# Performance work log

Hardware: AMD Instinct MI355X
Metric: run time of the kernel (lower is better)

Reference implementation:

```python
import jax, jax.numpy as jnp
import numpy as np

HEAD_SIZE = 64


def setup_inputs() -> dict:
    key = jax.random.key(0)
    k1, k2, k3, k4 = jax.random.split(key, 4)
    B, T, E = 8, 2048, 1024
    x = jax.random.normal(k1, (B, T, E), dtype=jnp.float32)
    # nn.Linear(n_embd, head_size, bias=False) weights: [head_size, n_embd]
    s = 1.0 / np.sqrt(E)
    Wk = jax.random.uniform(k2, (HEAD_SIZE, E), jnp.float32, -s, s)
    Wq = jax.random.uniform(k3, (HEAD_SIZE, E), jnp.float32, -s, s)
    Wv = jax.random.uniform(k4, (HEAD_SIZE, E), jnp.float32, -s, s)
    return {"x": x, "Wk": Wk, "Wq": Wq, "Wv": Wv}


def reference(x, Wk, Wq, Wv):
    # x: [B, T, E]; W*: [D, E] with D = head_size
    B, T, E = x.shape
    k = jnp.einsum("bte,de->btd", x, Wk)  # [B,T,D]
    q = jnp.einsum("bte,de->btd", x, Wq)
    v = jnp.einsum("bte,de->btd", x, Wv)
    scale = k.shape[-1] ** -0.5
    wei = jnp.einsum("btd,bsd->bts", q, k) * scale  # [B,T,T]
    causal = jnp.tril(jnp.ones((T, T), dtype=bool))
    wei = jnp.where(causal, wei, -jnp.inf)
    wei = jax.nn.softmax(wei, axis=-1)
    # dropout p=0.0 (eval): identity
    return jnp.einsum("bts,bsd->btd", wei, v)
```

## Files before the change

kernel.cpp:

```cpp
#include <hip/hip_runtime.h>
#include <hip/hip_bf16.h>


typedef __bf16 bf16x8 __attribute__((ext_vector_type(8)));
typedef float  f32x4  __attribute__((ext_vector_type(4)));

#define T_SEQ 2048
#define E_DIM 1024
#define D_HEAD 64
#define M_TOT 16384

__device__ __forceinline__ unsigned short f2b(float f) {
  union { float f; unsigned int u; } cv; cv.f = f;
  unsigned int u = cv.u;
  u += 0x7FFFu + ((u >> 16) & 1u);
  return (unsigned short)(u >> 16);
}

__device__ __forceinline__ void dma16(const unsigned short* g, unsigned short* l) {
  __builtin_amdgcn_global_load_lds(
      (const __attribute__((address_space(1))) void*)g,
      (__attribute__((address_space(3))) void*)l, 16, 0, 0);
}

__global__ __launch_bounds__(256) void wcvt_kernel(
    const float* __restrict__ Wk, const float* __restrict__ Wq,
    const float* __restrict__ Wv, unsigned short* __restrict__ Wb)
{
  int i = blockIdx.x * 256 + threadIdx.x;
  int n = i >> 8, c4 = i & 255;
  const float* src = (n < 64) ? Wq + n * E_DIM
                   : (n < 128) ? Wk + (n - 64) * E_DIM
                               : Wv + (n - 128) * E_DIM;
  float4 v = *(const float4*)(src + c4 * 4);
  *(ushort4*)(Wb + (size_t)n * E_DIM + c4 * 4) =
      make_ushort4(f2b(v.x), f2b(v.y), f2b(v.z), f2b(v.w));
}

__global__ __launch_bounds__(256) void proj_kernel(
    const float* __restrict__ x, const unsigned short* __restrict__ Wb,
    unsigned short* __restrict__ qws, unsigned short* __restrict__ kws,
    unsigned short* __restrict__ vtws)
{
  __shared__ unsigned short x_lds[32 * 128];
  __shared__ unsigned short w_lds[192 * 128];

  const int tid = threadIdx.x, wv = tid >> 6, lane = tid & 63;
  const int c = lane & 15, quad = lane >> 4;
  const int row0 = blockIdx.x * 32;
  const int mi = wv & 1, nh = wv >> 1;

  f32x4 acc[6];
  for (int j = 0; j < 6; ++j)
    for (int r = 0; r < 4; ++r) acc[j][r] = 0.0f;

  for (int step = 0; step < 8; ++step) {
    const int k0 = step * 128;
    __syncthreads();
    for (int jj = 0; jj < 4; ++jj) {
      int idx = tid + jj * 256;
      int r = idx >> 5, h = idx & 31;
      float4 v = *(const float4*)(x + (size_t)(row0 + r) * E_DIM + k0 + h * 4);
      int pc = (h >> 1) ^ (r & 7);
      *(ushort4*)&x_lds[r * 128 + pc * 8 + (h & 1) * 4] =
          make_ushort4(f2b(v.x), f2b(v.y), f2b(v.z), f2b(v.w));
    }
    for (int j = 0; j < 12; ++j) {
      int base = (wv * 12 + j) * 64;
      int p = base + lane;
      int n = p >> 4, pg = p & 15, g = pg ^ (n & 7);
      dma16(Wb + (size_t)n * E_DIM + k0 + g * 8, &w_lds[base * 8]);
    }
    __syncthreads();
    const int m = mi * 16 + c;
    for (int ks = 0; ks < 4; ++ks) {
      int ga = (ks * 4 + quad) ^ (m & 7);
      bf16x8 a = *(const bf16x8*)&x_lds[m * 128 + ga * 8];
      for (int j = 0; j < 6; ++j) {
        int n = (nh * 6 + j) * 16 + c;
        int gb = (ks * 4 + quad) ^ (n & 7);
        bf16x8 bb = *(const bf16x8*)&w_lds[n * 128 + gb * 8];
        acc[j] = __builtin_amdgcn_mfma_f32_16x16x32_bf16(a, bb, acc[j], 0, 0, 0);
      }
    }
  }

  const int rbase = row0 + mi * 16 + quad * 4;
  for (int j = 0; j < 6; ++j) {
    int nt = nh * 6 + j;
    if (nt < 4) {
      int d = nt * 16 + c;
      for (int r = 0; r < 4; ++r) qws[(size_t)(rbase + r) * D_HEAD + d] = f2b(acc[j][r]);
    } else if (nt < 8) {
      int d = (nt - 4) * 16 + c;
      for (int r = 0; r < 4; ++r) kws[(size_t)(rbase + r) * D_HEAD + d] = f2b(acc[j][r]);
    } else {
      int d = (nt - 8) * 16 + c;
      int bb = rbase >> 11, tt = rbase & 2047;
      *(ushort4*)&vtws[(size_t)bb * D_HEAD * T_SEQ + (size_t)d * T_SEQ + tt] =
          make_ushort4(f2b(acc[j][0]), f2b(acc[j][1]), f2b(acc[j][2]), f2b(acc[j][3]));
    }
  }
}

__global__ __launch_bounds__(256) void attn_kernel(
    const unsigned short* __restrict__ qws, const unsigned short* __restrict__ kws,
    const unsigned short* __restrict__ vtws,
    float* __restrict__ opart, float* __restrict__ mpart, float* __restrict__ lpart)
{
  __shared__ unsigned short q_lds[64 * 64];
  __shared__ unsigned short k_lds[128 * 64];
  __shared__ unsigned short vt_lds[64 * 128];
  __shared__ unsigned short p_lds[64 * 128];

  const int tid = threadIdx.x, wv = tid >> 6, lane = tid & 63;
  const int c = lane & 15, quad = lane >> 4;
  const int qt = blockIdx.x, b = blockIdx.y, sg = blockIdx.z;
  const int t0 = qt * 64;
  const size_t qkbase = (size_t)b * T_SEQ * D_HEAD;
  const int ssmax = qt >> 1;
  const int niter = (ssmax >= sg) ? ((ssmax - sg) >> 1) + 1 : 0;
  const int rloc = wv * 16 + quad * 4;
  const size_t prow = ((size_t)sg * 8 + b) * T_SEQ;

  if (niter == 0) {
    for (int nt = 0; nt < 4; ++nt)
      for (int r = 0; r < 4; ++r)
        opart[(prow + t0 + rloc + r) * D_HEAD + nt * 16 + c] = 0.0f;
    if (c == 0)
      for (int r = 0; r < 4; ++r) {
        mpart[prow + t0 + rloc + r] = -__builtin_inff();
        lpart[prow + t0 + rloc + r] = 0.0f;
      }
    return;
  }

  for (int j = 0; j < 2; ++j) {
    int base = (wv * 2 + j) * 64;
    int p = base + lane;
    int r = p >> 3, pg = p & 7, g = pg ^ (r & 7);
    dma16(qws + qkbase + (size_t)(t0 + r) * D_HEAD + g * 8, &q_lds[base * 8]);
  }

  float m_st[4], l_st[4];
  f32x4 acc_o[4];
  for (int r = 0; r < 4; ++r) { m_st[r] = -__builtin_inff(); l_st[r] = 0.0f; }
  for (int nt = 0; nt < 4; ++nt)
    for (int r = 0; r < 4; ++r) acc_o[nt][r] = 0.0f;

  const float sc = 0.18033688011112042f;
  const int m_row = wv * 16 + c;

  for (int it = 0; it < niter; ++it) {
    const int ss = sg + 2 * it;
    const int s0 = ss * 128;
    __syncthreads();
    for (int j = 0; j < 4; ++j) {
      int base = (wv * 4 + j) * 64;
      int p = base + lane;
      int r = p >> 3, pg = p & 7, g = pg ^ (r & 7);
      dma16(kws + qkbase + (size_t)(s0 + r) * D_HEAD + g * 8, &k_lds[base * 8]);
    }
    for (int j = 0; j < 4; ++j) {
      int base = (wv * 4 + j) * 64;
      int p = base + lane;
      int r = p >> 4, pg = p & 15, g = pg ^ (r & 7);
      dma16(vtws + (size_t)b * D_HEAD * T_SEQ + (size_t)r * T_SEQ + s0 + g * 8,
            &vt_lds[base * 8]);
    }
    __syncthreads();

    f32x4 accs[8];
    for (int nt = 0; nt < 8; ++nt)
      for (int r = 0; r < 4; ++r) accs[nt][r] = 0.0f;
    for (int ks = 0; ks < 2; ++ks) {
      int ga = (ks * 4 + quad) ^ (m_row & 7);
      bf16x8 a = *(const bf16x8*)&q_lds[m_row * 64 + ga * 8];
      for (int nt = 0; nt < 8; ++nt) {
        int n = nt * 16 + c;
        int gb = (ks * 4 + quad) ^ (n & 7);
        bf16x8 bb = *(const bf16x8*)&k_lds[n * 64 + gb * 8];
        accs[nt] = __builtin_amdgcn_mfma_f32_16x16x32_bf16(a, bb, accs[nt], 0, 0, 0);
      }
    }
    for (int nt = 0; nt < 8; ++nt)
      for (int r = 0; r < 4; ++r) accs[nt][r] *= sc;
    if (ss == ssmax) {
      for (int nt = 0; nt < 8; ++nt) {
        int scol = s0 + nt * 16 + c;
        for (int r = 0; r < 4; ++r)
          if (scol > t0 + rloc + r) accs[nt][r] = -__builtin_inff();
      }
    }

    float mx[4];
    for (int r = 0; r < 4; ++r) {
      float v = accs[0][r];
      for (int nt = 1; nt < 8; ++nt) v = fmaxf(v, accs[nt][r]);
      mx[r] = v;
    }
    for (int off = 1; off < 16; off <<= 1)
      for (int r = 0; r < 4; ++r) mx[r] = fmaxf(mx[r], __shfl_xor(mx[r], off));
    float alpha[4], rsum[4];
    for (int r = 0; r < 4; ++r) {
      float mnew = fmaxf(m_st[r], mx[r]);
      alpha[r] = __builtin_exp2f(m_st[r] - mnew);
      m_st[r] = mnew;
      rsum[r] = 0.0f;
    }
    for (int nt = 0; nt < 8; ++nt)
      for (int r = 0; r < 4; ++r) {
        float p = __builtin_exp2f(accs[nt][r] - m_st[r]);
        accs[nt][r] = p;
        rsum[r] += p;
      }
    for (int off = 1; off < 16; off <<= 1)
      for (int r = 0; r < 4; ++r) rsum[r] += __shfl_xor(rsum[r], off);
    for (int r = 0; r < 4; ++r) l_st[r] = alpha[r] * l_st[r] + rsum[r];
    for (int nt = 0; nt < 4; ++nt)
      for (int r = 0; r < 4; ++r) acc_o[nt][r] *= alpha[r];

    for (int nt = 0; nt < 8; ++nt)
      for (int r = 0; r < 4; ++r) {
        int col = nt * 16 + c, rr = rloc + r;
        int pc = (col >> 3) ^ (rr & 7);
        p_lds[rr * 128 + pc * 8 + (col & 7)] = f2b(accs[nt][r]);
      }

    for (int ks = 0; ks < 4; ++ks) {
      int ga = (ks * 4 + quad) ^ (m_row & 7);
      bf16x8 a = *(const bf16x8*)&p_lds[m_row * 128 + ga * 8];
      for (int nt = 0; nt < 4; ++nt) {
        int n = nt * 16 + c;
        int gb = (ks * 4 + quad) ^ (n & 7);
        bf16x8 vv = *(const bf16x8*)&vt_lds[n * 128 + gb * 8];
        acc_o[nt] = __builtin_amdgcn_mfma_f32_16x16x32_bf16(a, vv, acc_o[nt], 0, 0, 0);
      }
    }
  }

  for (int nt = 0; nt < 4; ++nt)
    for (int r = 0; r < 4; ++r)
      opart[(prow + t0 + rloc + r) * D_HEAD + nt * 16 + c] = acc_o[nt][r];
  if (c == 0)
    for (int r = 0; r < 4; ++r) {
      mpart[prow + t0 + rloc + r] = m_st[r];
      lpart[prow + t0 + rloc + r] = l_st[r];
    }
}

__global__ __launch_bounds__(256) void merge_kernel(
    const float* __restrict__ opart, const float* __restrict__ mpart,
    const float* __restrict__ lpart, float* __restrict__ out)
{
  int gid = blockIdx.x * 256 + threadIdx.x;
  int gr = gid >> 4, q4 = gid & 15;
  float m0 = mpart[gr], m1 = mpart[M_TOT + gr];
  float l0 = lpart[gr], l1 = lpart[M_TOT + gr];
  float M = fmaxf(m0, m1);
  float w0 = __builtin_exp2f(m0 - M);
  float w1 = __builtin_exp2f(m1 - M);
  float inv = 1.0f / (w0 * l0 + w1 * l1);
  const float4 o0 = *(const float4*)(opart + (size_t)gr * D_HEAD + q4 * 4);
  const float4 o1 = *(const float4*)(opart + (size_t)M_TOT * D_HEAD + (size_t)gr * D_HEAD + q4 * 4);
  float4 o;
  o.x = (w0 * o0.x + w1 * o1.x) * inv;
  o.y = (w0 * o0.y + w1 * o1.y) * inv;
  o.z = (w0 * o0.z + w1 * o1.z) * inv;
  o.w = (w0 * o0.w + w1 * o1.w) * inv;
  *(float4*)(out + (size_t)gr * D_HEAD + q4 * 4) = o;
}

extern "C" void kernel_launch(void* const* d_in, const int* in_sizes, int n_in,
                              void* d_out, int out_size, void* d_ws, size_t ws_size,
                              hipStream_t stream) {
  const float* x  = (const float*)d_in[0];
  const float* Wk = (const float*)d_in[1];
  const float* Wq = (const float*)d_in[2];
  const float* Wv = (const float*)d_in[3];
  float* out = (float*)d_out;

  unsigned short* qws  = (unsigned short*)d_ws;
  unsigned short* kws  = qws + (size_t)M_TOT * D_HEAD;
  unsigned short* vtws = kws + (size_t)M_TOT * D_HEAD;
  unsigned short* Wb   = vtws + (size_t)M_TOT * D_HEAD;
  float* opart = (float*)(Wb + 192 * E_DIM);
  float* mpart = opart + 2 * (size_t)M_TOT * D_HEAD;
  float* lpart = mpart + 2 * (size_t)M_TOT;

  wcvt_kernel<<<192, 256, 0, stream>>>(Wk, Wq, Wv, Wb);
  proj_kernel<<<M_TOT / 32, 256, 0, stream>>>(x, Wb, qws, kws, vtws);
  attn_kernel<<<dim3(T_SEQ / 64, 8, 2), 256, 0, stream>>>(qws, kws, vtws, opart, mpart, lpart);
  merge_kernel<<<M_TOT * 16 / 256, 256, 0, stream>>>(opart, mpart, lpart, out);
}
```

Measured before the change: 144.8 us.

## Rewrite projection and attention to load fragments directly from global, split KV four ways

```diff
diff --git a/kernel.cpp b/kernel.cpp
--- a/kernel.cpp
+++ b/kernel.cpp
@@ -9,6 +9,8 @@
 #define E_DIM 1024
 #define D_HEAD 64
 #define M_TOT 16384
+#define NSPLIT 4
+#define SC_LOG2E 0.18033688011112042f
 
 __device__ __forceinline__ unsigned short f2b(float f) {
   union { float f; unsigned int u; } cv; cv.f = f;
@@ -17,10 +19,15 @@
   return (unsigned short)(u >> 16);
 }
 
-__device__ __forceinline__ void dma16(const unsigned short* g, unsigned short* l) {
-  __builtin_amdgcn_global_load_lds(
-      (const __attribute__((address_space(1))) void*)g,
-      (__attribute__((address_space(3))) void*)l, 16, 0, 0);
+__device__ __forceinline__ unsigned int f2b2(float a, float b) {
+#if __has_builtin(__builtin_amdgcn_cvt_pk_bf16_f32)
+  typedef __bf16 bf16x2_t __attribute__((ext_vector_type(2)));
+  union { bf16x2_t v; unsigned int u; } cv;
+  cv.v = __builtin_amdgcn_cvt_pk_bf16_f32(a, b);
+  return cv.u;
+#else
+  return (unsigned int)f2b(a) | ((unsigned int)f2b(b) << 16);
+#endif
 }
 
 __global__ __launch_bounds__(256) void wcvt_kernel(
@@ -33,100 +40,94 @@
                    : (n < 128) ? Wk + (n - 64) * E_DIM
                                : Wv + (n - 128) * E_DIM;
   float4 v = *(const float4*)(src + c4 * 4);
-  *(ushort4*)(Wb + (size_t)n * E_DIM + c4 * 4) =
-      make_ushort4(f2b(v.x), f2b(v.y), f2b(v.z), f2b(v.w));
-}
-
-__global__ __launch_bounds__(256) void proj_kernel(
+  unsigned int lo = f2b2(v.x, v.y), hi = f2b2(v.z, v.w);
+  *(uint2*)(Wb + (size_t)n * E_DIM + c4 * 4) = make_uint2(lo, hi);
+}
+
+__global__ __launch_bounds__(192) void proj_kernel(
     const float* __restrict__ x, const unsigned short* __restrict__ Wb,
     unsigned short* __restrict__ qws, unsigned short* __restrict__ kws,
     unsigned short* __restrict__ vtws)
 {
-  __shared__ unsigned short x_lds[32 * 128];
-  __shared__ unsigned short w_lds[192 * 128];
-
-  const int tid = threadIdx.x, wv = tid >> 6, lane = tid & 63;
+  const int tid = threadIdx.x, wv = tid / 64, lane = tid & 63;
   const int c = lane & 15, quad = lane >> 4;
-  const int row0 = blockIdx.x * 32;
-  const int mi = wv & 1, nh = wv >> 1;
-
-  f32x4 acc[6];
-  for (int j = 0; j < 6; ++j)
-    for (int r = 0; r < 4; ++r) acc[j][r] = 0.0f;
-
-  for (int step = 0; step < 8; ++step) {
-    const int k0 = step * 128;
-    __syncthreads();
-    for (int jj = 0; jj < 4; ++jj) {
-      int idx = tid + jj * 256;
-      int r = idx >> 5, h = idx & 31;
-      float4 v = *(const float4*)(x + (size_t)(row0 + r) * E_DIM + k0 + h * 4);
-      int pc = (h >> 1) ^ (r & 7);
-      *(ushort4*)&x_lds[r * 128 + pc * 8 + (h & 1) * 4] =
-          make_ushort4(f2b(v.x), f2b(v.y), f2b(v.z), f2b(v.w));
-    }
-    for (int j = 0; j < 12; ++j) {
-      int base = (wv * 12 + j) * 64;
-      int p = base + lane;
-      int n = p >> 4, pg = p & 15, g = pg ^ (n & 7);
-      dma16(Wb + (size_t)n * E_DIM + k0 + g * 8, &w_lds[base * 8]);
-    }
-    __syncthreads();
-    const int m = mi * 16 + c;
-    for (int ks = 0; ks < 4; ++ks) {
-      int ga = (ks * 4 + quad) ^ (m & 7);
-      bf16x8 a = *(const bf16x8*)&x_lds[m * 128 + ga * 8];
-      for (int j = 0; j < 6; ++j) {
-        int n = (nh * 6 + j) * 16 + c;
-        int gb = (ks * 4 + quad) ^ (n & 7);
-        bf16x8 bb = *(const bf16x8*)&w_lds[n * 128 + gb * 8];
-        acc[j] = __builtin_amdgcn_mfma_f32_16x16x32_bf16(a, bb, acc[j], 0, 0, 0);
-      }
-    }
-  }
-
-  const int rbase = row0 + mi * 16 + quad * 4;
-  for (int j = 0; j < 6; ++j) {
-    int nt = nh * 6 + j;
-    if (nt < 4) {
-      int d = nt * 16 + c;
-      for (int r = 0; r < 4; ++r) qws[(size_t)(rbase + r) * D_HEAD + d] = f2b(acc[j][r]);
-    } else if (nt < 8) {
-      int d = (nt - 4) * 16 + c;
-      for (int r = 0; r < 4; ++r) kws[(size_t)(rbase + r) * D_HEAD + d] = f2b(acc[j][r]);
+  const int mt0 = blockIdx.x * 2;
+  const int ng = wv;
+  const size_t xr0 = (size_t)(mt0 * 16 + c) * E_DIM + quad * 8;
+  const size_t xr1 = xr0 + 16 * E_DIM;
+
+  f32x4 acc0[4], acc1[4];
+  for (int j = 0; j < 4; ++j)
+    for (int r = 0; r < 4; ++r) { acc0[j][r] = 0.0f; acc1[j][r] = 0.0f; }
+
+  for (int k = 0; k < E_DIM; k += 32) {
+    union { unsigned int u32[4]; bf16x8 v8; } a0, a1;
+    {
+      float4 u = *(const float4*)(x + xr0 + k);
+      float4 w = *(const float4*)(x + xr0 + k + 4);
+      a0.u32[0] = f2b2(u.x, u.y); a0.u32[1] = f2b2(u.z, u.w);
+      a0.u32[2] = f2b2(w.x, w.y); a0.u32[3] = f2b2(w.z, w.w);
+    }
+    {
+      float4 u = *(const float4*)(x + xr1 + k);
+      float4 w = *(const float4*)(x + xr1 + k + 4);
+      a1.u32[0] = f2b2(u.x, u.y); a1.u32[1] = f2b2(u.z, u.w);
+      a1.u32[2] = f2b2(w.x, w.y); a1.u32[3] = f2b2(w.z, w.w);
+    }
+    for (int j = 0; j < 4; ++j) {
+      bf16x8 bb = *(const bf16x8*)(Wb + (size_t)(ng * 64 + j * 16 + c) * E_DIM + k + quad * 8);
+      acc0[j] = __builtin_amdgcn_mfma_f32_16x16x32_bf16(a0.v8, bb, acc0[j], 0, 0, 0);
+      acc1[j] = __builtin_amdgcn_mfma_f32_16x16x32_bf16(a1.v8, bb, acc1[j], 0, 0, 0);
+    }
+  }
+
+  for (int half = 0; half < 2; ++half) {
+    const f32x4* acc = half ? acc1 : acc0;
+    const int rbase = (mt0 + half) * 16 + quad * 4;
+    if (ng == 0) {
+      for (int j = 0; j < 4; ++j) {
+        int d = j * 16 + c;
+        for (int r = 0; r < 4; ++r)
+          qws[(size_t)(rbase + r) * D_HEAD + d] = f2b(acc[j][r] * SC_LOG2E);
+      }
+    } else if (ng == 1) {
+      for (int j = 0; j < 4; ++j) {
+        int d = j * 16 + c;
+        for (int r = 0; r < 4; ++r)
+          kws[(size_t)(rbase + r) * D_HEAD + d] = f2b(acc[j][r]);
+      }
     } else {
-      int d = (nt - 8) * 16 + c;
       int bb = rbase >> 11, tt = rbase & 2047;
-      *(ushort4*)&vtws[(size_t)bb * D_HEAD * T_SEQ + (size_t)d * T_SEQ + tt] =
-          make_ushort4(f2b(acc[j][0]), f2b(acc[j][1]), f2b(acc[j][2]), f2b(acc[j][3]));
-    }
-  }
-}
-
-__global__ __launch_bounds__(256) void attn_kernel(
+      for (int j = 0; j < 4; ++j) {
+        int d = j * 16 + c;
+        *(ushort4*)&vtws[(size_t)bb * D_HEAD * T_SEQ + (size_t)d * T_SEQ + tt] =
+            make_ushort4(f2b(acc[j][0]), f2b(acc[j][1]), f2b(acc[j][2]), f2b(acc[j][3]));
+      }
+    }
+  }
+}
+
+__global__ __launch_bounds__(256, 4) void attn_kernel(
     const unsigned short* __restrict__ qws, const unsigned short* __restrict__ kws,
     const unsigned short* __restrict__ vtws,
-    float* __restrict__ opart, float* __restrict__ mpart, float* __restrict__ lpart)
-{
-  __shared__ unsigned short q_lds[64 * 64];
-  __shared__ unsigned short k_lds[128 * 64];
-  __shared__ unsigned short vt_lds[64 * 128];
-  __shared__ unsigned short p_lds[64 * 128];
+    unsigned short* __restrict__ opart, float* __restrict__ mpart,
+    float* __restrict__ lpart)
+{
+  __shared__ __align__(16) unsigned short p_lds[64 * 64];
 
   const int tid = threadIdx.x, wv = tid >> 6, lane = tid & 63;
   const int c = lane & 15, quad = lane >> 4;
   const int qt = blockIdx.x, b = blockIdx.y, sg = blockIdx.z;
   const int t0 = qt * 64;
-  const size_t qkbase = (size_t)b * T_SEQ * D_HEAD;
-  const int ssmax = qt >> 1;
-  const int niter = (ssmax >= sg) ? ((ssmax - sg) >> 1) + 1 : 0;
+  const size_t qkb = (size_t)b * T_SEQ * D_HEAD;
+  const int niter = (qt >= sg) ? ((qt - sg) >> 2) + 1 : 0;
   const int rloc = wv * 16 + quad * 4;
   const size_t prow = ((size_t)sg * 8 + b) * T_SEQ;
 
   if (niter == 0) {
     for (int nt = 0; nt < 4; ++nt)
       for (int r = 0; r < 4; ++r)
-        opart[(prow + t0 + rloc + r) * D_HEAD + nt * 16 + c] = 0.0f;
+        opart[(prow + t0 + rloc + r) * D_HEAD + nt * 16 + c] = 0;
     if (c == 0)
       for (int r = 0; r < 4; ++r) {
         mpart[prow + t0 + rloc + r] = -__builtin_inff();
@@ -135,58 +136,39 @@
     return;
   }
 
-  for (int j = 0; j < 2; ++j) {
-    int base = (wv * 2 + j) * 64;
-    int p = base + lane;
-    int r = p >> 3, pg = p & 7, g = pg ^ (r & 7);
-    dma16(qws + qkbase + (size_t)(t0 + r) * D_HEAD + g * 8, &q_lds[base * 8]);
-  }
-
-  float m_st[4], l_st[4];
-  f32x4 acc_o[4];
-  for (int r = 0; r < 4; ++r) { m_st[r] = -__builtin_inff(); l_st[r] = 0.0f; }
+  const int mrow = wv * 16 + c;
+  const bf16x8 qf0 = *(const bf16x8*)(qws + qkb + (size_t)(t0 + mrow) * D_HEAD + quad * 8);
+  const bf16x8 qf1 = *(const bf16x8*)(qws + qkb + (size_t)(t0 + mrow) * D_HEAD + 32 + quad * 8);
+
+  bf16x8 ones;
+  { union { unsigned short s[8]; bf16x8 v; } o;
+    for (int i = 0; i < 8; ++i) o.s[i] = 0x3F80;
+    ones = o.v; }
+
+  float m_st[4];
+  f32x4 acc_o[4], acc_l;
+  for (int r = 0; r < 4; ++r) { m_st[r] = -__builtin_inff(); acc_l[r] = 0.0f; }
   for (int nt = 0; nt < 4; ++nt)
     for (int r = 0; r < 4; ++r) acc_o[nt][r] = 0.0f;
 
-  const float sc = 0.18033688011112042f;
-  const int m_row = wv * 16 + c;
+  const bool mydiag = (sg == (qt & 3));
 
   for (int it = 0; it < niter; ++it) {
-    const int ss = sg + 2 * it;
-    const int s0 = ss * 128;
-    __syncthreads();
-    for (int j = 0; j < 4; ++j) {
-      int base = (wv * 4 + j) * 64;
-      int p = base + lane;
-      int r = p >> 3, pg = p & 7, g = pg ^ (r & 7);
-      dma16(kws + qkbase + (size_t)(s0 + r) * D_HEAD + g * 8, &k_lds[base * 8]);
-    }
-    for (int j = 0; j < 4; ++j) {
-      int base = (wv * 4 + j) * 64;
-      int p = base + lane;
-      int r = p >> 4, pg = p & 15, g = pg ^ (r & 7);
-      dma16(vtws + (size_t)b * D_HEAD * T_SEQ + (size_t)r * T_SEQ + s0 + g * 8,
-            &vt_lds[base * 8]);
-    }
-    __syncthreads();
-
-    f32x4 accs[8];
-    for (int nt = 0; nt < 8; ++nt)
+    const int s0 = (sg + 4 * it) * 64;
+    const bool diag = mydiag && (it == niter - 1);
+
+    f32x4 accs[4];
+    for (int nt = 0; nt < 4; ++nt)
       for (int r = 0; r < 4; ++r) accs[nt][r] = 0.0f;
-    for (int ks = 0; ks < 2; ++ks) {
-      int ga = (ks * 4 + quad) ^ (m_row & 7);
-      bf16x8 a = *(const bf16x8*)&q_lds[m_row * 64 + ga * 8];
-      for (int nt = 0; nt < 8; ++nt) {
-        int n = nt * 16 + c;
-        int gb = (ks * 4 + quad) ^ (n & 7);
-        bf16x8 bb = *(const bf16x8*)&k_lds[n * 64 + gb * 8];
-        accs[nt] = __builtin_amdgcn_mfma_f32_16x16x32_bf16(a, bb, accs[nt], 0, 0, 0);
-      }
-    }
-    for (int nt = 0; nt < 8; ++nt)
-      for (int r = 0; r < 4; ++r) accs[nt][r] *= sc;
-    if (ss == ssmax) {
-      for (int nt = 0; nt < 8; ++nt) {
+    for (int nt = 0; nt < 4; ++nt) {
+      const unsigned short* kp = kws + qkb + (size_t)(s0 + nt * 16 + c) * D_HEAD + quad * 8;
+      bf16x8 k0 = *(const bf16x8*)kp;
+      bf16x8 k1 = *(const bf16x8*)(kp + 32);
+      accs[nt] = __builtin_amdgcn_mfma_f32_16x16x32_bf16(qf0, k0, accs[nt], 0, 0, 0);
+      accs[nt] = __builtin_amdgcn_mfma_f32_16x16x32_bf16(qf1, k1, accs[nt], 0, 0, 0);
+    }
+    if (diag) {
+      for (int nt = 0; nt < 4; ++nt) {
         int scol = s0 + nt * 16 + c;
         for (int r = 0; r < 4; ++r)
           if (scol > t0 + rloc + r) accs[nt][r] = -__builtin_inff();
@@ -194,81 +176,75 @@
     }
 
     float mx[4];
-    for (int r = 0; r < 4; ++r) {
-      float v = accs[0][r];
-      for (int nt = 1; nt < 8; ++nt) v = fmaxf(v, accs[nt][r]);
-      mx[r] = v;
-    }
+    for (int r = 0; r < 4; ++r)
+      mx[r] = fmaxf(fmaxf(accs[0][r], accs[1][r]), fmaxf(accs[2][r], accs[3][r]));
     for (int off = 1; off < 16; off <<= 1)
       for (int r = 0; r < 4; ++r) mx[r] = fmaxf(mx[r], __shfl_xor(mx[r], off));
-    float alpha[4], rsum[4];
+    float alpha[4];
     for (int r = 0; r < 4; ++r) {
       float mnew = fmaxf(m_st[r], mx[r]);
       alpha[r] = __builtin_exp2f(m_st[r] - mnew);
       m_st[r] = mnew;
-      rsum[r] = 0.0f;
-    }
-    for (int nt = 0; nt < 8; ++nt)
+    }
+    for (int nt = 0; nt < 4; ++nt)
+      for (int r = 0; r < 4; ++r)
+        accs[nt][r] = __builtin_exp2f(accs[nt][r] - m_st[r]);
+    for (int r = 0; r < 4; ++r) acc_l[r] *= alpha[r];
+    for (int nt = 0; nt < 4; ++nt)
+      for (int r = 0; r < 4; ++r) acc_o[nt][r] *= alpha[r];
+
+    for (int nt = 0; nt < 4; ++nt)
       for (int r = 0; r < 4; ++r) {
-        float p = __builtin_exp2f(accs[nt][r] - m_st[r]);
-        accs[nt][r] = p;
-        rsum[r] += p;
-      }
-    for (int off = 1; off < 16; off <<= 1)
-      for (int r = 0; r < 4; ++r) rsum[r] += __shfl_xor(rsum[r], off);
-    for (int r = 0; r < 4; ++r) l_st[r] = alpha[r] * l_st[r] + rsum[r];
-    for (int nt = 0; nt < 4; ++nt)
-      for (int r = 0; r < 4; ++r) acc_o[nt][r] *= alpha[r];
-
-    for (int nt = 0; nt < 8; ++nt)
-      for (int r = 0; r < 4; ++r) {
-        int col = nt * 16 + c, rr = rloc + r;
-        int pc = (col >> 3) ^ (rr & 7);
-        p_lds[rr * 128 + pc * 8 + (col & 7)] = f2b(accs[nt][r]);
-      }
-
-    for (int ks = 0; ks < 4; ++ks) {
-      int ga = (ks * 4 + quad) ^ (m_row & 7);
-      bf16x8 a = *(const bf16x8*)&p_lds[m_row * 128 + ga * 8];
+        int rr = rloc + r;
+        p_lds[rr * 64 + (((nt * 2 + (c >> 3)) ^ (rr & 7)) << 3) + (c & 7)] = f2b(accs[nt][r]);
+      }
+
+    for (int ks = 0; ks < 2; ++ks) {
+      int kg = ks * 4 + quad;
+      bf16x8 pf = *(const bf16x8*)&p_lds[mrow * 64 + ((kg ^ (mrow & 7)) << 3)];
+      acc_l = __builtin_amdgcn_mfma_f32_16x16x32_bf16(pf, ones, acc_l, 0, 0, 0);
       for (int nt = 0; nt < 4; ++nt) {
-        int n = nt * 16 + c;
-        int gb = (ks * 4 + quad) ^ (n & 7);
-        bf16x8 vv = *(const bf16x8*)&vt_lds[n * 128 + gb * 8];
-        acc_o[nt] = __builtin_amdgcn_mfma_f32_16x16x32_bf16(a, vv, acc_o[nt], 0, 0, 0);
+        const bf16x8 vv = *(const bf16x8*)(vtws + (size_t)b * D_HEAD * T_SEQ +
+                                           (size_t)(nt * 16 + c) * T_SEQ + s0 + ks * 32 + quad * 8);
+        acc_o[nt] = __builtin_amdgcn_mfma_f32_16x16x32_bf16(pf, vv, acc_o[nt], 0, 0, 0);
       }
     }
   }
 
   for (int nt = 0; nt < 4; ++nt)
     for (int r = 0; r < 4; ++r)
-      opart[(prow + t0 + rloc + r) * D_HEAD + nt * 16 + c] = acc_o[nt][r];
+      opart[(prow + t0 + rloc + r) * D_HEAD + nt * 16 + c] = f2b(acc_o[nt][r]);
   if (c == 0)
     for (int r = 0; r < 4; ++r) {
       mpart[prow + t0 + rloc + r] = m_st[r];
-      lpart[prow + t0 + rloc + r] = l_st[r];
+      lpart[prow + t0 + rloc + r] = acc_l[r];
     }
 }
 
 __global__ __launch_bounds__(256) void merge_kernel(
-    const float* __restrict__ opart, const float* __restrict__ mpart,
+    const unsigned short* __restrict__ opart, const float* __restrict__ mpart,
     const float* __restrict__ lpart, float* __restrict__ out)
 {
   int gid = blockIdx.x * 256 + threadIdx.x;
-  int gr = gid >> 4, q4 = gid & 15;
-  float m0 = mpart[gr], m1 = mpart[M_TOT + gr];
-  float l0 = lpart[gr], l1 = lpart[M_TOT + gr];
-  float M = fmaxf(m0, m1);
-  float w0 = __builtin_exp2f(m0 - M);
-  float w1 = __builtin_exp2f(m1 - M);
-  float inv = 1.0f / (w0 * l0 + w1 * l1);
-  const float4 o0 = *(const float4*)(opart + (size_t)gr * D_HEAD + q4 * 4);
-  const float4 o1 = *(const float4*)(opart + (size_t)M_TOT * D_HEAD + (size_t)gr * D_HEAD + q4 * 4);
-  float4 o;
-  o.x = (w0 * o0.x + w1 * o1.x) * inv;
-  o.y = (w0 * o0.y + w1 * o1.y) * inv;
-  o.z = (w0 * o0.z + w1 * o1.z) * inv;
-  o.w = (w0 * o0.w + w1 * o1.w) * inv;
-  *(float4*)(out + (size_t)gr * D_HEAD + q4 * 4) = o;
+  int gr = gid >> 4, d4 = (gid & 15) * 4;
+  float m[NSPLIT], M = -__builtin_inff();
+  for (int i = 0; i < NSPLIT; ++i) { m[i] = mpart[(size_t)i * M_TOT + gr]; M = fmaxf(M, m[i]); }
+  float L = 0.0f, w[NSPLIT];
+  for (int i = 0; i < NSPLIT; ++i) {
+    w[i] = __builtin_exp2f(m[i] - M);
+    L += w[i] * lpart[(size_t)i * M_TOT + gr];
+  }
+  float inv = 1.0f / L;
+  float4 o = make_float4(0.f, 0.f, 0.f, 0.f);
+  for (int i = 0; i < NSPLIT; ++i) {
+    ushort4 u = *(const ushort4*)(opart + (size_t)i * M_TOT * D_HEAD + (size_t)gr * D_HEAD + d4);
+    union { unsigned int u; float f; } cx, cy, cz, cw;
+    cx.u = (unsigned int)u.x << 16; cy.u = (unsigned int)u.y << 16;
+    cz.u = (unsigned int)u.z << 16; cw.u = (unsigned int)u.w << 16;
+    o.x += w[i] * cx.f; o.y += w[i] * cy.f; o.z += w[i] * cz.f; o.w += w[i] * cw.f;
+  }
+  o.x *= inv; o.y *= inv; o.z *= inv; o.w *= inv;
+  *(float4*)(out + (size_t)gr * D_HEAD + d4) = o;
 }
 
 extern "C" void kernel_launch(void* const* d_in, const int* in_sizes, int n_in,
@@ -280,16 +256,16 @@
   const float* Wv = (const float*)d_in[3];
   float* out = (float*)d_out;
 
-  unsigned short* qws  = (unsigned short*)d_ws;
-  unsigned short* kws  = qws + (size_t)M_TOT * D_HEAD;
-  unsigned short* vtws = kws + (size_t)M_TOT * D_HEAD;
-  unsigned short* Wb   = vtws + (size_t)M_TOT * D_HEAD;
-  float* opart = (float*)(Wb + 192 * E_DIM);
-  float* mpart = opart + 2 * (size_t)M_TOT * D_HEAD;
-  float* lpart = mpart + 2 * (size_t)M_TOT;
+  unsigned short* qws   = (unsigned short*)d_ws;
+  unsigned short* kws   = qws + (size_t)M_TOT * D_HEAD;
+  unsigned short* vtws  = kws + (size_t)M_TOT * D_HEAD;
+  unsigned short* Wb    = vtws + (size_t)M_TOT * D_HEAD;
+  unsigned short* opart = Wb + 192 * E_DIM;
+  float* mpart = (float*)(opart + (size_t)NSPLIT * M_TOT * D_HEAD);
+  float* lpart = mpart + (size_t)NSPLIT * M_TOT;
 
   wcvt_kernel<<<192, 256, 0, stream>>>(Wk, Wq, Wv, Wb);
-  proj_kernel<<<M_TOT / 32, 256, 0, stream>>>(x, Wb, qws, kws, vtws);
-  attn_kernel<<<dim3(T_SEQ / 64, 8, 2), 256, 0, stream>>>(qws, kws, vtws, opart, mpart, lpart);
+  proj_kernel<<<M_TOT / 32, 192, 0, stream>>>(x, Wb, qws, kws, vtws);
+  attn_kernel<<<dim3(T_SEQ / 64, 8, NSPLIT), 256, 0, stream>>>(qws, kws, vtws, opart, mpart, lpart);
   merge_kernel<<<M_TOT * 16 / 256, 256, 0, stream>>>(opart, mpart, lpart, out);
 }
```

After: 198.9 us. +37.3%, slower.
